# Kernel tuning notes

Measured on AMD Instinct MI355X. Metric: run time of the kernel, lower is better.

Reference implementation:

```python
import jax, jax.numpy as jnp
import numpy as np
from functools import partial

# Mask R-CNN inference-config constants
BBOX_STD_DEV = jnp.array([0.1, 0.1, 0.2, 0.2], dtype=jnp.float32)
DETECTION_MIN_CONFIDENCE = 0.7
DETECTION_NMS_THRESHOLD = 0.3
DETECTION_MAX_INSTANCES = 100
NUM_CLASSES = 81
CLASS_OFFSET = 2.0  # > max extent of normalized boxes -> zero cross-class IoU


def setup_inputs() -> dict:
    key = jax.random.key(0)
    k1, k2, k3, k4 = jax.random.split(key, 4)
    B, N, C = 8, 2000, NUM_CLASSES
    # normalized rois with y1<y2, x1<x2
    yx = jax.random.uniform(k1, (B, N, 2)) * 0.7
    hw = jax.random.uniform(k2, (B, N, 2)) * 0.25 + 0.01
    rois = jnp.concatenate([yx, yx + hw], axis=-1)
    # peaked class probabilities so many rois exceed the 0.7 confidence floor
    mrcnn_class = jax.nn.softmax(jax.random.normal(k3, (B, N, C)) * 5.0, axis=-1)
    mrcnn_bbox = jax.random.normal(k4, (B, N, C, 4)) * 0.5
    meta = np.zeros((B, 12 + C), dtype=np.float32)
    meta[:, 1:4] = [1024.0, 1024.0, 3.0]   # original_image_shape
    meta[:, 4:7] = [1024.0, 1024.0, 3.0]   # image_shape
    meta[:, 7:11] = [0.0, 0.0, 1024.0, 1024.0]  # window in pixels
    meta[:, 11] = 1.0                       # scale
    meta[:, 12:] = 1.0                      # active_class_ids
    return {"rois": rois, "mrcnn_class": mrcnn_class,
            "mrcnn_bbox": mrcnn_bbox, "image_meta": jnp.asarray(meta)}


def _apply_box_deltas(boxes, deltas):
    h = boxes[:, 2] - boxes[:, 0]
    w = boxes[:, 3] - boxes[:, 1]
    cy = boxes[:, 0] + 0.5 * h + deltas[:, 0] * h
    cx = boxes[:, 1] + 0.5 * w + deltas[:, 1] * w
    h = h * jnp.exp(deltas[:, 2])
    w = w * jnp.exp(deltas[:, 3])
    y1 = cy - 0.5 * h
    x1 = cx - 0.5 * w
    return jnp.stack([y1, x1, y1 + h, x1 + w], axis=1)


def _clip_boxes(boxes, window):
    wy1, wx1, wy2, wx2 = window[0], window[1], window[2], window[3]
    y1 = jnp.clip(boxes[:, 0], wy1, wy2)
    x1 = jnp.clip(boxes[:, 1], wx1, wx2)
    y2 = jnp.clip(boxes[:, 2], wy1, wy2)
    x2 = jnp.clip(boxes[:, 3], wx1, wx2)
    return jnp.stack([y1, x1, y2, x2], axis=1)


def _iou_matrix(b):
    y1, x1, y2, x2 = b[:, 0], b[:, 1], b[:, 2], b[:, 3]
    area = (y2 - y1) * (x2 - x1)
    ih = jnp.clip(jnp.minimum(y2[:, None], y2[None, :]) - jnp.maximum(y1[:, None], y1[None, :]), 0.0)
    iw = jnp.clip(jnp.minimum(x2[:, None], x2[None, :]) - jnp.maximum(x1[:, None], x1[None, :]), 0.0)
    inter = ih * iw
    union = area[:, None] + area[None, :] - inter
    return inter / (union + 1e-8)


def _refine_detections(rois, probs, deltas, window):
    N = probs.shape[0]
    class_ids = jnp.argmax(probs, axis=1)                       # [N]
    rng = jnp.arange(N)
    class_scores = probs[rng, class_ids]
    deltas_specific = deltas[rng, class_ids]                    # [N,4]
    refined = _apply_box_deltas(rois, deltas_specific * BBOX_STD_DEV)
    refined = _clip_boxes(refined, window)
    valid = (class_ids > 0) & (class_scores >= DETECTION_MIN_CONFIDENCE)
    # sort by score desc (invalid pushed to the end)
    order = jnp.argsort(-jnp.where(valid, class_scores, -1.0))
    boxes_s = refined[order]
    # per-class NMS via class-offset trick: IoU across classes is exactly 0
    offset = class_ids[order].astype(refined.dtype)[:, None] * CLASS_OFFSET
    iou = jax.lax.stop_gradient(_iou_matrix(boxes_s + offset))
    keep0 = valid[order]
    idxs = jnp.arange(N)

    def body(i, keep):
        sup = (iou[i] > DETECTION_NMS_THRESHOLD) & keep[i] & (idxs > i)
        return keep & ~sup

    keep = jax.lax.fori_loop(0, N, body, keep0)
    sel_scores = jnp.where(keep, class_scores[order], -1.0)
    top_vals, top_i = jax.lax.top_k(sel_scores, DETECTION_MAX_INSTANCES)
    mask = (top_vals >= 0.0).astype(refined.dtype)[:, None]
    idx = order[top_i]
    det = jnp.concatenate([
        refined[idx],
        class_ids[idx].astype(refined.dtype)[:, None],
        class_scores[idx][:, None],
    ], axis=1)
    return det * mask                                           # [100,6], zero-padded


def reference(rois, mrcnn_class, mrcnn_bbox, image_meta):
    image_shape = image_meta[0, 4:7]
    h, w = image_shape[0], image_shape[1]
    scale = jnp.stack([h, w, h, w]) - 1.0
    shift = jnp.array([0.0, 0.0, 1.0, 1.0], dtype=image_meta.dtype)
    window = (image_meta[:, 7:11] - shift) / scale              # [B,4] normalized
    return jax.vmap(_refine_detections)(rois, mrcnn_class, mrcnn_bbox, window)
```

## Files before the change

### kernel.cpp

```cpp
#include <hip/hip_runtime.h>
#include <cfloat>
#include <cmath>

#define NROI 2000
#define NCLS 81
#define META 93
#define NMS_TAU 0.3f
#define MINCONF 0.7f
#define MAXDET 100
#define SORTN 2048

typedef unsigned long long u64;


__global__ __launch_bounds__(256) void refine_kernel(const float* __restrict__ rois,
                                                     const float* __restrict__ probs,
                                                     const float* __restrict__ deltas,
                                                     const float* __restrict__ meta,
                                                     float4* __restrict__ wbox,
                                                     u64* __restrict__ wpack,
                                                     int total) {
#pragma clang fp contract(off)
    const int tid = threadIdx.x;
    const int r = tid & 7;
    const int t = blockIdx.x * 32 + (tid >> 3);
    if (t >= total) return;
    const int b = t / NROI;
    const int j = t - b * NROI;

    const float* p = probs + (size_t)t * NCLS;
    float best = p[r];
    int bi = r;
    for (int c = r + 8; c < NCLS; c += 8) {
        float v = p[c];
        if (v > best) { best = v; bi = c; }
    }
    for (int m = 1; m < 8; m <<= 1) {
        float v2 = __shfl_xor(best, m);
        int i2 = __shfl_xor(bi, m);
        if (v2 > best || (v2 == best && i2 < bi)) { best = v2; bi = i2; }
    }
    if (r != 0) return;

    const float* dp = deltas + ((size_t)t * NCLS + bi) * 4;
    float4 dd = *(const float4*)dp;
    float d0 = dd.x * 0.1f, d1 = dd.y * 0.1f, d2 = dd.z * 0.2f, d3 = dd.w * 0.2f;
    float4 rr = *(const float4*)(rois + (size_t)t * 4);
    float r0 = rr.x, r1 = rr.y, r2 = rr.z, r3 = rr.w;
    float h = r2 - r0, w = r3 - r1;
    float cy = (r0 + 0.5f * h) + d0 * h;
    float cx = (r1 + 0.5f * w) + d1 * w;
    float h2 = h * expf(d2);
    float w2 = w * expf(d3);
    float y1 = cy - 0.5f * h2, x1 = cx - 0.5f * w2;
    float y2 = y1 + h2, x2 = x1 + w2;

    const float sy = meta[4] - 1.0f;
    const float sx = meta[5] - 1.0f;
    const float* mb = meta + (size_t)b * META;
    const float wy1 = (mb[7] - 0.0f) / sy;
    const float wx1 = (mb[8] - 0.0f) / sx;
    const float wy2 = (mb[9] - 1.0f) / sy;
    const float wx2 = (mb[10] - 1.0f) / sx;
    y1 = fminf(fmaxf(y1, wy1), wy2);
    x1 = fminf(fmaxf(x1, wx1), wx2);
    y2 = fminf(fmaxf(y2, wy1), wy2);
    x2 = fminf(fmaxf(x2, wx1), wx2);

    bool valid = (bi > 0) && (best >= MINCONF);
    float key = valid ? best : -1.0f;
    unsigned kb = __float_as_uint(key);
    unsigned ip = (kb & 0x80000000u) ? ~kb : (kb | 0x80000000u);
    unsigned dk = ~ip;
    wbox[t] = make_float4(y1, x1, y2, x2);
    wpack[(size_t)b * SORTN + j] = ((u64)dk << 32) | (unsigned)(j << 7) | (unsigned)bi;
}

__global__ __launch_bounds__(512) void sort512_kernel(u64* __restrict__ wpack) {
    __shared__ u64 sp[512];
    const int bc = blockIdx.x;
    const int b = bc >> 2, chunk = bc & 3;
    const int base = chunk * 512;
    const int tid = threadIdx.x;

    int j = base + tid;
    u64 v = (j < NROI) ? wpack[(size_t)b * SORTN + j]
                       : (0xC000000000000000ull | (u64)((unsigned)j << 7));

    for (int k = 2; k <= 512; k <<= 1) {
        const bool asc = ((tid & k) == 0);
        for (int jj = k >> 1; jj > 0; jj >>= 1) {
            u64 pv;
            if (jj >= 64) {
                sp[tid] = v;
                __syncthreads();
                pv = sp[tid ^ jj];
                __syncthreads();
            } else {
                pv = __shfl_xor(v, jj);
            }
            bool lower = ((tid & jj) == 0);
            bool keepmin = (lower == asc);
            bool vless = (v < pv);
            v = (keepmin == vless) ? v : pv;
        }
    }
    wpack[(size_t)b * SORTN + base + tid] = v;
}

__global__ __launch_bounds__(1024) void merge_nms_kernel(const float4* __restrict__ wbox,
                                                         const u64* __restrict__ wpack,
                                                         float* __restrict__ out) {
#pragma clang fp contract(off)
    __shared__ u64 s_pack[SORTN];
    __shared__ float4 s_boxArena[NROI];
    __shared__ unsigned char s_keep[SORTN];
    __shared__ float s_cy1[64], s_cx1[64], s_cy2[64], s_cx2[64], s_car[64];
    __shared__ int s_ccl[64], s_init[64];
    __shared__ u64 s_sup[64];
    __shared__ u64 s_clsmask[NCLS];
    __shared__ u64 s_alive;
    __shared__ int s_scan[17];
    __shared__ int s_total, s_V;

    u64* s_tmp = (u64*)s_boxArena;
    float4* s_box = s_boxArena;

    const int b = blockIdx.x;
    const int tid = threadIdx.x;

    float4 rb0 = wbox[b * NROI + tid];
    float4 rb1;
    const int bj1 = tid + 1024;
    if (bj1 < NROI) rb1 = wbox[b * NROI + bj1];

    for (int j = tid; j < SORTN; j += 1024)
        s_pack[j] = wpack[(size_t)b * SORTN + j];
    __syncthreads();

    for (int i = tid; i < SORTN; i += 1024) {
        u64 x = s_pack[i];
        int run = i >> 9, local = i & 511;
        int pbase = (run ^ 1) << 9;
        int lo = 0, hi = 512;
        while (lo < hi) {
            int mid = (lo + hi) >> 1;
            if (s_pack[pbase + mid] < x) lo = mid + 1; else hi = mid;
        }
        s_tmp[((run >> 1) << 10) + local + lo] = x;
    }
    __syncthreads();

    for (int i = tid; i < SORTN; i += 1024) {
        u64 x = s_tmp[i];
        int run = i >> 10, local = i & 1023;
        int pbase = (run ^ 1) << 10;
        int lo = 0, hi = 1024;
        while (lo < hi) {
            int mid = (lo + hi) >> 1;
            if (s_tmp[pbase + mid] < x) lo = mid + 1; else hi = mid;
        }
        s_pack[local + lo] = x;
    }
    __syncthreads();

    s_box[tid] = rb0;
    if (bj1 < NROI) s_box[bj1] = rb1;
    if (tid == 0) {
        int lo = 0, hi = SORTN;
        while (lo < hi) {
            int mid = (lo + hi) >> 1;
            if (!(s_pack[mid] >> 63)) lo = mid + 1; else hi = mid;
        }
        s_V = lo;
        s_total = 0;
    }
    __syncthreads();
    const int V = s_V;
    for (int j = tid; j < SORTN; j += 1024) s_keep[j] = (j < V) ? 1 : 0;
    __syncthreads();

    for (int c = 0; c < V; c += 64) {
        bool init_flag = false;
        if (tid < 64) {
            int j = c + tid;
            int cl = -1;
            float y1 = 0.f, x1 = 0.f, y2 = 0.f, x2 = 0.f, ar = 0.f;
            if (j < V) {
                init_flag = (s_keep[j] != 0);
                u64 pk = s_pack[j];
                int o = (int)((pk >> 7) & 0x7FF);
                cl = (int)(pk & 0x7F);
                float4 bx = s_box[o];
                float off = (float)cl * 2.0f;
                y1 = bx.x + off; x1 = bx.y + off; y2 = bx.z + off; x2 = bx.w + off;
                ar = (y2 - y1) * (x2 - x1);
            }
            s_cy1[tid] = y1; s_cx1[tid] = x1; s_cy2[tid] = y2; s_cx2[tid] = x2;
            s_car[tid] = ar; s_ccl[tid] = cl; s_init[tid] = init_flag ? 1 : 0;
        } else if (tid >= 64 && tid < 64 + NCLS) {
            s_clsmask[tid - 64] = 0ull;
        }
        __syncthreads();

        {
            int i = tid & 63;
            int w = tid >> 6;
            float iy1 = s_cy1[i], ix1 = s_cx1[i], iy2 = s_cy2[i], ix2 = s_cx2[i];
            float iar = s_car[i];
            int icl = s_ccl[i], iin = s_init[i];
#pragma unroll
            for (int p = 0; p < 4; ++p) {
                int jr = w + (p << 4);
                float jy1 = s_cy1[jr], jx1 = s_cx1[jr], jy2 = s_cy2[jr], jx2 = s_cx2[jr];
                float jar = s_car[jr];
                int jcl = s_ccl[jr], jin = s_init[jr];
                bool bit = false;
                if (i < jr && iin && jin && icl == jcl) {
                    float ih = fmaxf(fminf(jy2, iy2) - fmaxf(jy1, iy1), 0.0f);
                    float iw = fmaxf(fminf(jx2, ix2) - fmaxf(jx1, ix1), 0.0f);
                    float inter = ih * iw;
                    float iou = inter / ((jar + iar - inter) + 1e-8f);
                    bit = iou > NMS_TAU;
                }
                u64 m = __ballot(bit);
                if (i == 0) s_sup[jr] = m;
            }
        }
        __syncthreads();

        if (tid < 64) {
            u64 sup = s_sup[tid];
            u64 initm = __ballot(init_flag);
            u64 hasup = __ballot(init_flag && sup != 0ull);
            u64 alive = initm & ~hasup;
            u64 m = hasup;
            while (m) {
                int t2 = __ffsll((unsigned long long)m) - 1;
                m &= m - 1;
                u64 st = __shfl(sup, t2);
                if ((st & alive) == 0ull) alive |= (1ull << t2);
            }
            s_keep[c + tid] = (unsigned char)((alive >> tid) & 1ull);
            if ((alive >> tid) & 1ull)
                atomicOr(&s_clsmask[s_ccl[tid]], 1ull << tid);
            if (tid == 0) { s_alive = alive; s_total += __popcll(alive); }
        }
        __syncthreads();
        if (s_total >= MAXDET) break;

        if (s_alive) {
            for (int j = c + 64 + tid; j < V; j += 1024) {
                if (!s_keep[j]) continue;
                u64 pk = s_pack[j];
                int myc = (int)(pk & 0x7F);
                u64 m = s_clsmask[myc];
                if (!m) continue;
                int o = (int)((pk >> 7) & 0x7FF);
                float4 bx = s_box[o];
                float off = (float)myc * 2.0f;
                float y1 = bx.x + off, x1 = bx.y + off, y2 = bx.z + off, x2 = bx.w + off;
                float ar = (y2 - y1) * (x2 - x1);
                int keep = 1;
                while (m) {
                    int kI = __ffsll((unsigned long long)m) - 1;
                    m &= m - 1;
                    float iy1 = s_cy1[kI], ix1 = s_cx1[kI];
                    float iy2 = s_cy2[kI], ix2 = s_cx2[kI];
                    float iar = s_car[kI];
                    float ih = fmaxf(fminf(y2, iy2) - fmaxf(y1, iy1), 0.0f);
                    float iw = fmaxf(fminf(x2, ix2) - fmaxf(x1, ix1), 0.0f);
                    float inter = ih * iw;
                    float iou = inter / ((ar + iar - inter) + 1e-8f);
                    if (iou > NMS_TAU) { keep = 0; break; }
                }
                if (!keep) s_keep[j] = 0;
            }
        }
        __syncthreads();
    }
    __syncthreads();

    int a0 = (int)s_keep[2 * tid], a1 = (int)s_keep[2 * tid + 1];
    int ssum = a0 + a1;
    int lane = tid & 63, wid = tid >> 6;
    int v = ssum;
    for (int off = 1; off < 64; off <<= 1) {
        int n = __shfl_up(v, off);
        if (lane >= off) v += n;
    }
    if (lane == 63) s_scan[wid] = v;
    __syncthreads();
    if (tid == 0) {
        int acc = 0;
        for (int wv = 0; wv < 16; ++wv) { int t2 = s_scan[wv]; s_scan[wv] = acc; acc += t2; }
        s_scan[16] = acc;
    }
    __syncthreads();
    int incl = v + s_scan[wid];
    int excl0 = incl - ssum;
    int excl1 = excl0 + a0;

    float* ob = out + (size_t)b * (MAXDET * 6);
    for (int e = 0; e < 2; ++e) {
        int j = 2 * tid + e;
        int kp = e ? a1 : a0;
        int rk = e ? excl1 : excl0;
        if (kp && rk < MAXDET) {
            u64 pk = s_pack[j];
            int o = (int)((pk >> 7) & 0x7FF);
            int cl = (int)(pk & 0x7F);
            unsigned ip = ~(unsigned)(pk >> 32);
            unsigned kb = (ip & 0x80000000u) ? (ip & 0x7FFFFFFFu) : ~ip;
            float4 bx = s_box[o];
            float* row = ob + rk * 6;
            row[0] = bx.x; row[1] = bx.y; row[2] = bx.z; row[3] = bx.w;
            row[4] = (float)cl;
            row[5] = __uint_as_float(kb);
        }
    }
    int K = s_scan[16];
    if (K > MAXDET) K = MAXDET;
    for (int s0 = K + tid; s0 < MAXDET; s0 += 1024) {
        float* row = ob + s0 * 6;
#pragma unroll
        for (int q = 0; q < 6; ++q) row[q] = 0.0f;
    }
}

__global__ __launch_bounds__(1024) void det_kernel(const float* __restrict__ rois,
                                                   const float* __restrict__ probs,
                                                   const float* __restrict__ deltas,
                                                   const float* __restrict__ meta,
                                                   float* __restrict__ out) {
#pragma clang fp contract(off)
    __shared__ float s_key[SORTN];
    __shared__ unsigned short s_idx[SORTN];
    __shared__ float4 s_box[NROI];
    __shared__ unsigned char s_cls[NROI];
    __shared__ unsigned char s_keep[SORTN];
    __shared__ float s_chunk[64 * 5];
    __shared__ int s_scan[17];
    __shared__ int s_nk, s_total, s_V;

    const int b = blockIdx.x;
    const int tid = threadIdx.x;

    const float sy = meta[4] - 1.0f;
    const float sx = meta[5] - 1.0f;
    const float* mb = meta + (size_t)b * META;
    const float wy1 = (mb[7] - 0.0f) / sy;
    const float wx1 = (mb[8] - 0.0f) / sx;
    const float wy2 = (mb[9] - 1.0f) / sy;
    const float wx2 = (mb[10] - 1.0f) / sx;

    for (int j = tid; j < SORTN; j += 1024) {
        s_idx[j] = (unsigned short)j;
        if (j >= NROI) { s_key[j] = -2.0f; continue; }
        const int t = b * NROI + j;
        const float* p = probs + (size_t)t * NCLS;
        float best = p[0];
        int bi = 0;
        for (int c = 1; c < NCLS; ++c) {
            float v = p[c];
            if (v > best) { best = v; bi = c; }
        }
        const float* dp = deltas + ((size_t)t * NCLS + bi) * 4;
        float d0 = dp[0] * 0.1f, d1 = dp[1] * 0.1f, d2 = dp[2] * 0.2f, d3 = dp[3] * 0.2f;
        const float* rp = rois + (size_t)t * 4;
        float r0 = rp[0], r1 = rp[1], r2 = rp[2], r3 = rp[3];
        float h = r2 - r0, w = r3 - r1;
        float cy = (r0 + 0.5f * h) + d0 * h;
        float cx = (r1 + 0.5f * w) + d1 * w;
        float h2 = h * expf(d2);
        float w2 = w * expf(d3);
        float y1 = cy - 0.5f * h2, x1 = cx - 0.5f * w2;
        float y2 = y1 + h2, x2 = x1 + w2;
        y1 = fminf(fmaxf(y1, wy1), wy2);
        x1 = fminf(fmaxf(x1, wx1), wx2);
        y2 = fminf(fmaxf(y2, wy1), wy2);
        x2 = fminf(fmaxf(x2, wx1), wx2);
        bool valid = (bi > 0) && (best >= MINCONF);
        s_key[j] = valid ? best : -1.0f;
        s_box[j] = make_float4(y1, x1, y2, x2);
        s_cls[j] = (unsigned char)bi;
    }
    __syncthreads();

    for (int k = 2; k <= SORTN; k <<= 1) {
        for (int jj = k >> 1; jj > 0; jj >>= 1) {
            for (int i = tid; i < SORTN; i += 1024) {
                int ixj = i ^ jj;
                if (ixj > i) {
                    float ka = s_key[i], kb = s_key[ixj];
                    unsigned short ia = s_idx[i], ib = s_idx[ixj];
                    bool b_prec_a = (kb > ka) || (kb == ka && ib < ia);
                    bool dir = ((i & k) == 0);
                    if (b_prec_a == dir) {
                        s_key[i] = kb; s_key[ixj] = ka;
                        s_idx[i] = ib; s_idx[ixj] = ia;
                    }
                }
            }
            __syncthreads();
        }
    }

    if (tid == 0) {
        int lo = 0, hi = SORTN;
        while (lo < hi) {
            int mid = (lo + hi) >> 1;
            if (s_key[mid] > 0.0f) lo = mid + 1; else hi = mid;
        }
        s_V = lo;
        s_total = 0;
    }
    __syncthreads();
    const int V = s_V;

    for (int j = tid; j < SORTN; j += 1024) s_keep[j] = (j < V) ? 1 : 0;
    __syncthreads();

    for (int c = 0; c < V; c += 64) {
        if (tid < 64) {
            int j = c + tid;
            int keep = 0;
            float y1 = 0.f, x1 = 0.f, y2 = 0.f, x2 = 0.f, ar = 0.f;
            if (j < V) {
                keep = (int)s_keep[j];
                int o = (int)s_idx[j];
                float4 bx = s_box[o];
                float off = (float)s_cls[o] * 2.0f;
                y1 = bx.x + off; x1 = bx.y + off; y2 = bx.z + off; x2 = bx.w + off;
                ar = (y2 - y1) * (x2 - x1);
            }
            for (int i = 0; i < 63; ++i) {
                int ki = __shfl(keep, i);
                float iy1 = __shfl(y1, i), ix1 = __shfl(x1, i);
                float iy2 = __shfl(y2, i), ix2 = __shfl(x2, i);
                float iar = __shfl(ar, i);
                if (tid > i && keep && ki) {
                    float ih = fmaxf(fminf(y2, iy2) - fmaxf(y1, iy1), 0.0f);
                    float iw = fmaxf(fminf(x2, ix2) - fmaxf(x1, ix1), 0.0f);
                    float inter = ih * iw;
                    float iou = inter / ((ar + iar - inter) + 1e-8f);
                    if (iou > NMS_TAU) keep = 0;
                }
            }
            if (j < V) s_keep[j] = (unsigned char)keep;
            unsigned long long bal = __ballot(keep && (j < V));
            int nk = __popcll(bal);
            if (keep && j < V) {
                int pos = __popcll(bal & ((1ULL << tid) - 1ULL));
                s_chunk[pos * 5 + 0] = y1; s_chunk[pos * 5 + 1] = x1;
                s_chunk[pos * 5 + 2] = y2; s_chunk[pos * 5 + 3] = x2;
                s_chunk[pos * 5 + 4] = ar;
            }
            if (tid == 0) { s_nk = nk; s_total += nk; }
        }
        __syncthreads();
        if (s_total >= MAXDET) break;
        int nk = s_nk;
        if (nk > 0) {
            for (int j = c + 64 + tid; j < V; j += 1024) {
                if (!s_keep[j]) continue;
                int o = (int)s_idx[j];
                float4 bx = s_box[o];
                float off = (float)s_cls[o] * 2.0f;
                float y1 = bx.x + off, x1 = bx.y + off, y2 = bx.z + off, x2 = bx.w + off;
                float ar = (y2 - y1) * (x2 - x1);
                int keep = 1;
                for (int kI = 0; kI < nk; ++kI) {
                    float iy1 = s_chunk[kI * 5 + 0], ix1 = s_chunk[kI * 5 + 1];
                    float iy2 = s_chunk[kI * 5 + 2], ix2 = s_chunk[kI * 5 + 3];
                    float iar = s_chunk[kI * 5 + 4];
                    float ih = fmaxf(fminf(y2, iy2) - fmaxf(y1, iy1), 0.0f);
                    float iw = fmaxf(fminf(x2, ix2) - fmaxf(x1, ix1), 0.0f);
                    float inter = ih * iw;
                    float iou = inter / ((ar + iar - inter) + 1e-8f);
                    if (iou > NMS_TAU) { keep = 0; break; }
                }
                if (!keep) s_keep[j] = 0;
            }
        }
        __syncthreads();
    }
    __syncthreads();

    int a0 = (int)s_keep[2 * tid], a1 = (int)s_keep[2 * tid + 1];
    int ssum = a0 + a1;
    int lane = tid & 63, wid = tid >> 6;
    int v = ssum;
    for (int off = 1; off < 64; off <<= 1) {
        int n = __shfl_up(v, off);
        if (lane >= off) v += n;
    }
    if (lane == 63) s_scan[wid] = v;
    __syncthreads();
    if (tid == 0) {
        int acc = 0;
        for (int wv = 0; wv < 16; ++wv) { int t2 = s_scan[wv]; s_scan[wv] = acc; acc += t2; }
        s_scan[16] = acc;
    }
    __syncthreads();
    int incl = v + s_scan[wid];
    int excl0 = incl - ssum;
    int excl1 = excl0 + a0;

    float* ob = out + (size_t)b * (MAXDET * 6);
    for (int e = 0; e < 2; ++e) {
        int j = 2 * tid + e;
        int kp = e ? a1 : a0;
        int rk = e ? excl1 : excl0;
        if (kp && rk < MAXDET) {
            int o = (int)s_idx[j];
            float4 bx = s_box[o];
            float* row = ob + rk * 6;
            row[0] = bx.x; row[1] = bx.y; row[2] = bx.z; row[3] = bx.w;
            row[4] = (float)s_cls[o];
            row[5] = s_key[j];
        }
    }
    int K = s_scan[16];
    if (K > MAXDET) K = MAXDET;
    for (int s0 = K + tid; s0 < MAXDET; s0 += 1024) {
        float* row = ob + s0 * 6;
#pragma unroll
        for (int q = 0; q < 6; ++q) row[q] = 0.0f;
    }
}

extern "C" void kernel_launch(void* const* d_in, const int* in_sizes, int n_in,
                              void* d_out, int out_size, void* d_ws, size_t ws_size,
                              hipStream_t stream) {
    const float* rois   = (const float*)d_in[0];
    const float* probs  = (const float*)d_in[1];
    const float* deltas = (const float*)d_in[2];
    const float* meta   = (const float*)d_in[3];
    float* out = (float*)d_out;

    int B = in_sizes[0] / (NROI * 4);
    int total = B * NROI;

    size_t need = (size_t)total * 16 + (size_t)B * SORTN * 8;
    if (ws_size >= need) {
        float4* wbox = (float4*)d_ws;
        u64*    wpack = (u64*)(wbox + total);
        refine_kernel<<<(total + 31) / 32, 256, 0, stream>>>(rois, probs, deltas, meta,
                                                             wbox, wpack, total);
        sort512_kernel<<<B * 4, 512, 0, stream>>>(wpack);
        merge_nms_kernel<<<B, 1024, 0, stream>>>(wbox, wpack, out);
    } else {
        det_kernel<<<B, 1024, 0, stream>>>(rois, probs, deltas, meta, out);
    }
}
```

Before: 94.79 us.

## Fold per-chunk bitonic sort into NMS kernel with register sort and merge passes

Removes the separate sort512 kernel launch. Inside the merge/NMS kernel, each wavefront now sorts 128 keys in registers using shuffles (two keys per lane), and four shared-memory merge-path passes (run lengths 128 to 1024) produce the full sorted order. This saves a kernel launch and a global round trip of the packed keys. In exchange it adds two extra binary-search merge passes inside a kernel that runs on only B blocks.

```diff
diff --git a/kernel.cpp b/kernel.cpp
--- a/kernel.cpp
+++ b/kernel.cpp
@@ -12,6 +12,7 @@
 
 typedef unsigned long long u64;
 
+#define PADPACK(j) (0xC000000000000000ull | (u64)((unsigned)(j) << 7))
 
 __global__ __launch_bounds__(256) void refine_kernel(const float* __restrict__ rois,
                                                      const float* __restrict__ probs,
@@ -76,38 +77,6 @@
     wpack[(size_t)b * SORTN + j] = ((u64)dk << 32) | (unsigned)(j << 7) | (unsigned)bi;
 }
 
-__global__ __launch_bounds__(512) void sort512_kernel(u64* __restrict__ wpack) {
-    __shared__ u64 sp[512];
-    const int bc = blockIdx.x;
-    const int b = bc >> 2, chunk = bc & 3;
-    const int base = chunk * 512;
-    const int tid = threadIdx.x;
-
-    int j = base + tid;
-    u64 v = (j < NROI) ? wpack[(size_t)b * SORTN + j]
-                       : (0xC000000000000000ull | (u64)((unsigned)j << 7));
-
-    for (int k = 2; k <= 512; k <<= 1) {
-        const bool asc = ((tid & k) == 0);
-        for (int jj = k >> 1; jj > 0; jj >>= 1) {
-            u64 pv;
-            if (jj >= 64) {
-                sp[tid] = v;
-                __syncthreads();
-                pv = sp[tid ^ jj];
-                __syncthreads();
-            } else {
-                pv = __shfl_xor(v, jj);
-            }
-            bool lower = ((tid & jj) == 0);
-            bool keepmin = (lower == asc);
-            bool vless = (v < pv);
-            v = (keepmin == vless) ? v : pv;
-        }
-    }
-    wpack[(size_t)b * SORTN + base + tid] = v;
-}
-
 __global__ __launch_bounds__(1024) void merge_nms_kernel(const float4* __restrict__ wbox,
                                                          const u64* __restrict__ wpack,
                                                          float* __restrict__ out) {
@@ -128,41 +97,67 @@
 
     const int b = blockIdx.x;
     const int tid = threadIdx.x;
+    const int lane = tid & 63;
+    const int wv = tid >> 6;
 
     float4 rb0 = wbox[b * NROI + tid];
     float4 rb1;
     const int bj1 = tid + 1024;
     if (bj1 < NROI) rb1 = wbox[b * NROI + bj1];
 
-    for (int j = tid; j < SORTN; j += 1024)
-        s_pack[j] = wpack[(size_t)b * SORTN + j];
-    __syncthreads();
-
-    for (int i = tid; i < SORTN; i += 1024) {
-        u64 x = s_pack[i];
-        int run = i >> 9, local = i & 511;
-        int pbase = (run ^ 1) << 9;
-        int lo = 0, hi = 512;
-        while (lo < hi) {
-            int mid = (lo + hi) >> 1;
-            if (s_pack[pbase + mid] < x) lo = mid + 1; else hi = mid;
-        }
-        s_tmp[((run >> 1) << 10) + local + lo] = x;
-    }
-    __syncthreads();
-
-    for (int i = tid; i < SORTN; i += 1024) {
-        u64 x = s_tmp[i];
-        int run = i >> 10, local = i & 1023;
-        int pbase = (run ^ 1) << 10;
-        int lo = 0, hi = 1024;
-        while (lo < hi) {
-            int mid = (lo + hi) >> 1;
-            if (s_tmp[pbase + mid] < x) lo = mid + 1; else hi = mid;
-        }
-        s_pack[local + lo] = x;
-    }
-    __syncthreads();
+    const u64* wp = wpack + (size_t)b * SORTN;
+    const int g0 = (wv << 7) + (lane << 1);
+    const int g1 = g0 + 1;
+    u64 v0, v1;
+    if (wv < 15) {
+        ulonglong2 ld = *(const ulonglong2*)(wp + g0);
+        v0 = ld.x; v1 = ld.y;
+    } else {
+        v0 = (g0 < NROI) ? wp[g0] : PADPACK(g0);
+        v1 = (g1 < NROI) ? wp[g1] : PADPACK(g1);
+    }
+
+    for (int k = 2; k <= 128; k <<= 1) {
+        const bool asc = ((lane & (k >> 1)) == 0);
+        for (int jj = k >> 1; jj >= 2; jj >>= 1) {
+            const int d = jj >> 1;
+            u64 p0 = __shfl_xor(v0, d);
+            u64 p1 = __shfl_xor(v1, d);
+            const bool lower = ((lane & d) == 0);
+            const bool keepmin = (lower == asc);
+            v0 = ((v0 < p0) == keepmin) ? v0 : p0;
+            v1 = ((v1 < p1) == keepmin) ? v1 : p1;
+        }
+        u64 lo = (v0 < v1) ? v0 : v1;
+        u64 hi = (v0 < v1) ? v1 : v0;
+        v0 = asc ? lo : hi;
+        v1 = asc ? hi : lo;
+    }
+    s_pack[g0] = v0;
+    s_pack[g1] = v1;
+    __syncthreads();
+
+    {
+        u64* src = s_pack;
+        u64* dst = s_tmp;
+#pragma unroll
+        for (int s = 7; s <= 10; ++s) {
+            const int L = 1 << s;
+            for (int i = tid; i < SORTN; i += 1024) {
+                u64 x = src[i];
+                int run = i >> s, local = i & (L - 1);
+                int pbase = (run ^ 1) << s;
+                int lo = 0, hi = L;
+                while (lo < hi) {
+                    int mid = (lo + hi) >> 1;
+                    if (src[pbase + mid] < x) lo = mid + 1; else hi = mid;
+                }
+                dst[((run >> 1) << (s + 1)) + local + lo] = x;
+            }
+            __syncthreads();
+            u64* t2 = src; src = dst; dst = t2;
+        }
+    }
 
     s_box[tid] = rb0;
     if (bj1 < NROI) s_box[bj1] = rb1;
@@ -283,7 +278,7 @@
 
     int a0 = (int)s_keep[2 * tid], a1 = (int)s_keep[2 * tid + 1];
     int ssum = a0 + a1;
-    int lane = tid & 63, wid = tid >> 6;
+    int wid = tid >> 6;
     int v = ssum;
     for (int off = 1; off < 64; off <<= 1) {
         int n = __shfl_up(v, off);
@@ -293,7 +288,7 @@
     __syncthreads();
     if (tid == 0) {
         int acc = 0;
-        for (int wv = 0; wv < 16; ++wv) { int t2 = s_scan[wv]; s_scan[wv] = acc; acc += t2; }
+        for (int w2 = 0; w2 < 16; ++w2) { int t2 = s_scan[w2]; s_scan[w2] = acc; acc += t2; }
         s_scan[16] = acc;
     }
     __syncthreads();
@@ -548,7 +543,6 @@
         u64*    wpack = (u64*)(wbox + total);
         refine_kernel<<<(total + 31) / 32, 256, 0, stream>>>(rois, probs, deltas, meta,
                                                              wbox, wpack, total);
-        sort512_kernel<<<B * 4, 512, 0, stream>>>(wpack);
         merge_nms_kernel<<<B, 1024, 0, stream>>>(wbox, wpack, out);
     } else {
         det_kernel<<<B, 1024, 0, stream>>>(rois, probs, deltas, meta, out);
```

After: 95.01 us. No clear change (+0.2%).
